# Kernel tuning notes

Measured on AMD Instinct MI355X. Metric: run time of the kernel, lower is better.

The kernel has to match this reference:

```python
import jax, jax.numpy as jnp
import numpy as np

B, S, H = 2, 2048, 2048
NH, NKV, HD = 16, 4, 128
ROPE_BASE = 10000.0


def setup_inputs() -> dict:
    key = jax.random.key(0)
    ks = jax.random.split(key, 5)
    x = jax.random.normal(ks[0], (B, S, H), dtype=jnp.float32)
    position_ids = jnp.arange(S, dtype=jnp.int64 if jax.config.jax_enable_x64 else jnp.int32).reshape(1, S)
    # Linear weights stored as [in, out] (equivalent to torch weight.T)
    sc = 1.0 / np.sqrt(H)
    Wq = jax.random.normal(ks[1], (H, NH * HD), dtype=jnp.float32) * sc
    Wk = jax.random.normal(ks[2], (H, NKV * HD), dtype=jnp.float32) * sc
    Wv = jax.random.normal(ks[3], (H, NKV * HD), dtype=jnp.float32) * sc
    Wo = jax.random.normal(ks[4], (NH * HD, H), dtype=jnp.float32) * (1.0 / np.sqrt(NH * HD))
    return {"x": x, "position_ids": position_ids, "Wq": Wq, "Wk": Wk, "Wv": Wv, "Wo": Wo}


def _rope(q, k, position_ids):
    # q: [B,S,NH,HD], k: [B,S,NKV,HD]; Llama-style half-split RoPE
    half = HD // 2
    inv_freq = 1.0 / (ROPE_BASE ** (jnp.arange(0, half, dtype=jnp.float32) * 2.0 / HD))
    ang = position_ids.astype(jnp.float32)[..., None] * inv_freq  # [b,S,half]
    cos = jnp.concatenate([jnp.cos(ang), jnp.cos(ang)], axis=-1)[:, :, None, :]  # [b,S,1,HD]
    sin = jnp.concatenate([jnp.sin(ang), jnp.sin(ang)], axis=-1)[:, :, None, :]

    def rot_half(t):
        t1, t2 = t[..., :half], t[..., half:]
        return jnp.concatenate([-t2, t1], axis=-1)

    return q * cos + rot_half(q) * sin, k * cos + rot_half(k) * sin


def reference(x, position_ids, Wq, Wk, Wv, Wo):
    b, s, _ = x.shape
    q = (x @ Wq).reshape(b, s, NH, HD)
    k = (x @ Wk).reshape(b, s, NKV, HD)
    v = (x @ Wv).reshape(b, s, NKV, HD)
    q, k = _rope(q, k, position_ids)
    reps = NH // NKV
    k = jnp.repeat(k, reps, axis=2)  # repeat_interleave on head dim
    v = jnp.repeat(v, reps, axis=2)
    q = q.transpose(0, 2, 1, 3)  # [b,h,s,d]
    k = k.transpose(0, 2, 1, 3)
    v = v.transpose(0, 2, 1, 3)
    scores = jnp.einsum('bhqd,bhkd->bhqk', q, k) / jnp.sqrt(jnp.float32(HD))
    causal = jnp.triu(jnp.ones((s, s), dtype=bool), k=1)
    scores = jnp.where(causal, -jnp.inf, scores)
    attn = jax.nn.softmax(scores.astype(jnp.float32), axis=-1).astype(q.dtype)
    out = jnp.einsum('bhqk,bhkd->bhqd', attn, v)
    out = out.transpose(0, 2, 1, 3).reshape(b, s, NH * HD)
    return out @ Wo
```

## Files before the change

kernel.cpp:

```cpp
#include <hip/hip_runtime.h>
#include <stdint.h>

typedef unsigned short u16;
typedef __attribute__((ext_vector_type(8))) short short8;
typedef __attribute__((ext_vector_type(4))) float floatx4;

#define S_LEN 2048
#define NQKV 3072

#if __has_builtin(__builtin_amdgcn_exp2f)
#define EXP2F __builtin_amdgcn_exp2f
#else
#define EXP2F exp2f
#endif

__device__ inline float bf2f(u16 u) {
  union { uint32_t u; float f; } v; v.u = ((uint32_t)u) << 16; return v.f;
}
__device__ inline u16 f2bf(float f) {
  union { float f; uint32_t u; } v; v.f = f;
  uint32_t r = v.u + 0x7fffu + ((v.u >> 16) & 1u);
  return (u16)(r >> 16);
}
__device__ inline void gl2lds16(const u16* g, u16* l) {
  __builtin_amdgcn_global_load_lds((const __attribute__((address_space(1))) uint32_t*)g,
                                   (__attribute__((address_space(3))) uint32_t*)l, 16, 0, 0);
}

__global__ void prep_k(const float* __restrict__ x, u16* __restrict__ Xb,
                       const float* __restrict__ Wq, const float* __restrict__ Wk,
                       const float* __restrict__ Wv, const float* __restrict__ Wo,
                       u16* __restrict__ WT, u16* __restrict__ WoT,
                       const int* __restrict__ pos, float2* __restrict__ rtab) {
  __shared__ u16 tile[32][33];
  const int b = blockIdx.x, t = threadIdx.x;
  if (b < 8192) {
    int i = b * 256 + t;
    float4 v = ((const float4*)x)[i];
    ushort4 o;
    o.x = f2bf(v.x); o.y = f2bf(v.y); o.z = f2bf(v.z); o.w = f2bf(v.w);
    ((ushort4*)Xb)[i] = o;
    return;
  }
  if (b >= 18432) {
    int i = (b - 18432) * 256 + t;
    int s = i >> 6, d = i & 63;
    float freq = __expf(-(float)d * 0.015625f * 9.210340371976184f);
    float ang = (float)pos[s] * freq;
    rtab[i] = make_float2(cosf(ang), sinf(ang));
    return;
  }
  int wb = b - 8192;
  const float* src; u16* dst; int bx, by;
  if (wb < 4096)      { src = Wq; dst = WT;                       bx = wb & 63;  by = wb >> 6; }
  else if (wb < 5120) { src = Wk; dst = WT + (size_t)2048 * 2048; bx = (wb - 4096) & 15; by = (wb - 4096) >> 4; }
  else if (wb < 6144) { src = Wv; dst = WT + (size_t)2560 * 2048; bx = (wb - 5120) & 15; by = (wb - 5120) >> 4; }
  else                { src = Wo; dst = WoT;                      bx = (wb - 6144) & 63; by = (wb - 6144) >> 6; }
  const int N = (wb >= 4096 && wb < 6144) ? 512 : 2048;
  int n0 = bx * 32, k0 = by * 32;
  int tx = t & 31, ty = t >> 5;
#pragma unroll
  for (int i = 0; i < 4; i++)
    tile[ty + 8 * i][tx] = f2bf(src[(size_t)(k0 + ty + 8 * i) * N + n0 + tx]);
  __syncthreads();
#pragma unroll
  for (int i = 0; i < 4; i++)
    dst[(size_t)(n0 + ty + 8 * i) * 2048 + k0 + tx] = tile[tx][ty + 8 * i];
}

__global__ void vtrans_k(const u16* __restrict__ qkv, u16* __restrict__ vt) {
  __shared__ u16 tile[32][33];
  int bk = blockIdx.x * 32, bd = blockIdx.y * 32, bz = blockIdx.z;
  int bb = bz >> 2, kvh = bz & 3;
  const u16* src = qkv + ((size_t)bb * S_LEN) * NQKV + 2560 + kvh * 128;
  u16* dst = vt + (size_t)bz * 128 * 2048;
  int tx = threadIdx.x, ty = threadIdx.y;
#pragma unroll
  for (int i = 0; i < 4; i++)
    tile[ty + 8 * i][tx] = src[(size_t)(bk + ty + 8 * i) * NQKV + bd + tx];
  __syncthreads();
#pragma unroll
  for (int i = 0; i < 4; i++)
    dst[(size_t)(bd + ty + 8 * i) * 2048 + bk + tx] = tile[tx][ty + 8 * i];
}

template <bool OUTF32>
__global__ __launch_bounds__(256) void gemm_bt(const u16* __restrict__ A, const u16* __restrict__ Bt,
                                               void* __restrict__ Cv, int M, int N, int K) {
  __shared__ u16 As[128 * 32];
  __shared__ u16 Bs[128 * 32];
  const int m0 = blockIdx.y * 128, n0 = blockIdx.x * 128;
  const int t = threadIdx.x, w = t >> 6, lane = t & 63;
  const int quad = lane >> 4, l16 = lane & 15;
  const int wm = (w >> 1) * 64, wn = (w & 1) * 64;
  const int lrow = lane >> 2, lk = (lane & 3) * 8;
  floatx4 acc[4][4] = {};
  for (int k0 = 0; k0 < K; k0 += 32) {
#pragma unroll
    for (int c = 2 * w; c <= 2 * w + 1; ++c) {
      int row = c * 16 + lrow;
      gl2lds16(A + (size_t)(m0 + row) * K + k0 + lk, As + c * 512 + lane * 8);
      gl2lds16(Bt + (size_t)(n0 + row) * K + k0 + lk, Bs + c * 512 + lane * 8);
    }
    __syncthreads();
    short8 a[4], b[4];
#pragma unroll
    for (int mt = 0; mt < 4; mt++) a[mt] = *(const short8*)(As + (wm + mt * 16 + l16) * 32 + quad * 8);
#pragma unroll
    for (int nt = 0; nt < 4; nt++) b[nt] = *(const short8*)(Bs + (wn + nt * 16 + l16) * 32 + quad * 8);
#pragma unroll
    for (int mt = 0; mt < 4; mt++)
#pragma unroll
      for (int nt = 0; nt < 4; nt++)
        acc[mt][nt] = __builtin_amdgcn_mfma_f32_16x16x32_bf16(a[mt], b[nt], acc[mt][nt], 0, 0, 0);
    __syncthreads();
  }
#pragma unroll
  for (int mt = 0; mt < 4; mt++)
#pragma unroll
    for (int nt = 0; nt < 4; nt++)
#pragma unroll
      for (int r = 0; r < 4; r++) {
        int row = m0 + wm + mt * 16 + quad * 4 + r;
        int col = n0 + wn + nt * 16 + l16;
        if (OUTF32)
          ((float*)Cv)[(size_t)row * N + col] = acc[mt][nt][r];
        else
          ((u16*)Cv)[(size_t)row * N + col] = f2bf(acc[mt][nt][r]);
      }
}

__global__ __launch_bounds__(512, 2) void gemm256_k(const u16* __restrict__ A,
                                                    const u16* __restrict__ Bt,
                                                    u16* __restrict__ C,
                                                    const float2* __restrict__ rtab,
                                                    int N, int K) {
  __shared__ u16 Al[2][2][8192];
  __shared__ u16 Bl[2][2][8192];
  const int TN = N >> 8;
  int flat = blockIdx.x;
  const int cpx = gridDim.x >> 3;
  flat = (flat & 7) * cpx + (flat >> 3);
  const int m0 = (flat / TN) << 8, n0 = (flat % TN) << 8;
  const int t = threadIdx.x, w = t >> 6, lane = t & 63;
  const int quad = lane >> 4, l16 = lane & 15;
  const int wm = w >> 2, wn = w & 3;
  const int sr = t >> 3, sl = t & 7;
  floatx4 acc[2][2][4][2] = {};
  const int NKT = K >> 6;

  const int ra_l = wm * 64 + l16;
  const int rb_l = wn * 16 + l16;

#pragma unroll
  for (int round = 0; round < 2; round++) {
    int r = round * 64 + sr;
    int so = (sl ^ (r & 7)) << 3;
    gl2lds16(A + (size_t)(m0 + r) * K + so, &Al[0][0][0] + round * 4096 + t * 8);
    gl2lds16(Bt + (size_t)(n0 + r) * K + so, &Bl[0][0][0] + round * 4096 + t * 8);
    gl2lds16(Bt + (size_t)(n0 + 128 + r) * K + so, &Bl[0][1][0] + round * 4096 + t * 8);
    gl2lds16(A + (size_t)(m0 + 128 + r) * K + so, &Al[0][1][0] + round * 4096 + t * 8);
  }
  asm volatile("s_waitcnt vmcnt(0)" ::: "memory");
  __builtin_amdgcn_s_barrier();

  short8 af[4][2];
  short8 bf[2][2][2];

  for (int kt = 0; kt < NKT; kt++) {
    const int c = kt & 1;
    const u16* Ab = &Al[c][0][0];
    const u16* Bb = &Bl[c][0][0];
    u16* An = &Al[c ^ 1][0][0];
    u16* Bn = &Bl[c ^ 1][0][0];
    const int k1 = (kt + 1) << 6;
    const bool pf = (kt + 1 < NKT);
#pragma unroll
    for (int ph = 0; ph < 4; ph++) {
      const int mh = (ph >> 1);
      const int nh = (ph == 1 || ph == 2) ? 1 : 0;
      if (ph == 0 || ph == 2) {
#pragma unroll
        for (int mt = 0; mt < 4; mt++) {
          int ra = ra_l + mt * 16;
          const u16* base = Ab + mh * 8192 + ra * 64;
#pragma unroll
          for (int ks = 0; ks < 2; ks++)
            af[mt][ks] = *(const short8*)(base + (((ks * 4 + quad) ^ (ra & 7)) << 3));
        }
      }
      if (ph == 0 || ph == 1) {
#pragma unroll
        for (int nt = 0; nt < 2; nt++) {
          int rb = rb_l + nt * 64;
          const u16* base = Bb + nh * 8192 + rb * 64;
#pragma unroll
          for (int ks = 0; ks < 2; ks++)
            bf[nh][nt][ks] = *(const short8*)(base + (((ks * 4 + quad) ^ (rb & 7)) << 3));
        }
      }
      if (pf) {
        const u16* G;
        u16* L;
        int rbase;
        if (ph == 0)      { G = A;  L = An;        rbase = m0; }
        else if (ph == 1) { G = Bt; L = Bn;        rbase = n0; }
        else if (ph == 2) { G = Bt; L = Bn + 8192; rbase = n0 + 128; }
        else              { G = A;  L = An + 8192; rbase = m0 + 128; }
#pragma unroll
        for (int round = 0; round < 2; round++) {
          int r = round * 64 + sr;
          gl2lds16(G + (size_t)(rbase + r) * K + k1 + ((sl ^ (r & 7)) << 3),
                   L + round * 4096 + t * 8);
        }
      }
      __builtin_amdgcn_s_barrier();
      asm volatile("s_waitcnt lgkmcnt(0)" ::: "memory");
      __builtin_amdgcn_s_setprio(1);
#pragma unroll
      for (int mt = 0; mt < 4; mt++)
#pragma unroll
        for (int nt = 0; nt < 2; nt++)
#pragma unroll
          for (int ks = 0; ks < 2; ks++)
            acc[mh][nh][mt][nt] =
                __builtin_amdgcn_mfma_f32_16x16x32_bf16(af[mt][ks], bf[nh][nt][ks], acc[mh][nh][mt][nt], 0, 0, 0);
      __builtin_amdgcn_s_setprio(0);
      if (ph != 2) asm volatile("s_waitcnt vmcnt(4)" ::: "memory");
      __builtin_amdgcn_s_barrier();
    }
  }
  const bool dorope = (n0 < 2560);
  const int dloc = wn * 16 + l16;
#pragma unroll
  for (int mh = 0; mh < 2; mh++)
#pragma unroll
    for (int mt = 0; mt < 4; mt++)
#pragma unroll
      for (int r = 0; r < 4; r++) {
        int row = m0 + mh * 128 + wm * 64 + mt * 16 + quad * 4 + r;
        float cc = 1.f, sn = 0.f;
        if (dorope) {
          float2 cs = rtab[(row & (S_LEN - 1)) * 64 + dloc];
          cc = cs.x; sn = cs.y;
        }
#pragma unroll
        for (int nh = 0; nh < 2; nh++) {
          float a0 = acc[mh][nh][mt][0][r], a1 = acc[mh][nh][mt][1][r];
          float o0 = dorope ? (a0 * cc - a1 * sn) : a0;
          float o1 = dorope ? (a1 * cc + a0 * sn) : a1;
          int colb = n0 + nh * 128 + wn * 16 + l16;
          C[(size_t)row * N + colb]      = f2bf(o0);
          C[(size_t)row * N + colb + 64] = f2bf(o1);
        }
      }
}

__global__ __launch_bounds__(256) void attn_k(const u16* __restrict__ qkv,
                                              const u16* __restrict__ vt,
                                              u16* __restrict__ ctx) {
  __shared__ u16 Kl[2][64 * 128];
  __shared__ u16 Vl[2][128 * 64];
  const int p = blockIdx.x;
  const int h = blockIdx.y, bb = blockIdx.z;
  const int kvh = h >> 2;
  const int t = threadIdx.x, w = t >> 6, lane = t & 63;
  const int quad = lane >> 4, l16 = lane & 15;
  const int sx = l16 & 7;
  const int kslot = lane & 15;
  const int vd0 = w * 32 + (lane >> 3);
  const int vslot = lane & 7;
  const int grow0 = (w & 1) * 4 + (w >> 1) * 32 + quad;
  const size_t rowbase = (size_t)bb * S_LEN;
  const u16* Kg0 = qkv + rowbase * NQKV + 2048 + kvh * 128;
  const u16* Vg0 = vt + (size_t)(bb * 4 + kvh) * 128 * 2048;
  const float c2 = 0.12751744f;
  short8 onesf = {16256, 16256, 16256, 16256, 16256, 16256, 16256, 16256};

  for (int phase = 0; phase < 2; phase++) {
    const int qt = phase ? p : 31 - p;
    const int rw = qt * 64 + w * 16;
    const int qrow = rw + l16;

    short8 qf[4];
#pragma unroll
    for (int ks = 0; ks < 4; ks++)
      qf[ks] = *(const short8*)(qkv + (rowbase + rw + l16) * NQKV + h * 128 + ks * 32 + quad * 8);

    floatx4 acc[8] = {};
    floatx4 accl = {0.f, 0.f, 0.f, 0.f};

    __syncthreads();
    {
#pragma unroll
      for (int ii = 0; ii < 4; ii++) {
        int p7 = (quad + 4 * ii) & 7;
        int grow = grow0 + 8 * ii;
        gl2lds16(Kg0 + (size_t)grow * NQKV + ((kslot ^ p7) * 8),
                 &Kl[0][0] + w * 2048 + ii * 512 + lane * 8);
      }
#pragma unroll
      for (int ii = 0; ii < 4; ii++) {
        int d = vd0 + ii * 8;
        gl2lds16(Vg0 + (size_t)d * 2048 + ((vslot ^ (d & 7)) * 8),
                 &Vl[0][0] + w * 2048 + ii * 512 + lane * 8);
      }
    }

    for (int kb = 0; kb <= qt; kb++) {
      const int cur = kb & 1;
      __builtin_amdgcn_s_barrier();
      if (kb < qt) {
        const u16* Kg = Kg0 + (size_t)(kb + 1) * 64 * NQKV;
        const u16* Vg = Vg0 + (kb + 1) * 64;
        u16* KlN = &Kl[cur ^ 1][0];
        u16* VlN = &Vl[cur ^ 1][0];
#pragma unroll
        for (int ii = 0; ii < 4; ii++) {
          int p7 = (quad + 4 * ii) & 7;
          int grow = grow0 + 8 * ii;
          gl2lds16(Kg + (size_t)grow * NQKV + ((kslot ^ p7) * 8),
                   KlN + w * 2048 + ii * 512 + lane * 8);
        }
#pragma unroll
        for (int ii = 0; ii < 4; ii++) {
          int d = vd0 + ii * 8;
          gl2lds16(Vg + (size_t)d * 2048 + ((vslot ^ (d & 7)) * 8),
                   VlN + w * 2048 + ii * 512 + lane * 8);
        }
        asm volatile("s_waitcnt vmcnt(8)" ::: "memory");
      } else {
        asm volatile("s_waitcnt vmcnt(0)" ::: "memory");
      }
      __builtin_amdgcn_s_barrier();
      const u16* KlB = &Kl[cur][0];
      const u16* VlB = &Vl[cur][0];

      floatx4 sc[4];
#pragma unroll
      for (int nt = 0; nt < 4; nt++) {
        const u16* Krow = KlB + (nt * 16 + l16) * 128;
        short8 kf[4];
#pragma unroll
        for (int ks = 0; ks < 4; ks++)
          kf[ks] = *(const short8*)(Krow + (((ks * 4 + quad) ^ sx) * 8));
        floatx4 s = {0.f, 0.f, 0.f, 0.f};
#pragma unroll
        for (int ks = 0; ks < 4; ks++) s = __builtin_amdgcn_mfma_f32_16x16x32_bf16(kf[ks], qf[ks], s, 0, 0, 0);
        sc[nt] = s;
      }
      const bool diag = (kb == qt);
      uint32_t pw[8];
#pragma unroll
      for (int nt = 0; nt < 4; nt++) {
        uint32_t w0 = 0, w1 = 0;
#pragma unroll
        for (int r = 0; r < 4; r++) {
          float e = EXP2F(sc[nt][r] * c2);
          if (diag) {
            int keyg = kb * 64 + quad * 8 + (nt & 1) * 4 + (nt >> 1) * 32 + r;
            if (keyg > qrow) e = 0.f;
          }
          uint32_t b = __float_as_uint(e) >> 16;
          if (r == 0) w0 = b;
          else if (r == 1) w0 |= b << 16;
          else if (r == 2) w1 = b;
          else w1 |= b << 16;
        }
        pw[nt * 2] = w0;
        pw[nt * 2 + 1] = w1;
      }
      union { short8 v; uint32_t u[4]; } pu0, pu1;
      pu0.u[0] = pw[0]; pu0.u[1] = pw[1]; pu0.u[2] = pw[2]; pu0.u[3] = pw[3];
      pu1.u[0] = pw[4]; pu1.u[1] = pw[5]; pu1.u[2] = pw[6]; pu1.u[3] = pw[7];
      const short8 pf0 = pu0.v, pf1 = pu1.v;

      accl = __builtin_amdgcn_mfma_f32_16x16x32_bf16(pf0, onesf, accl, 0, 0, 0);
      accl = __builtin_amdgcn_mfma_f32_16x16x32_bf16(pf1, onesf, accl, 0, 0, 0);
#pragma unroll
      for (int nto = 0; nto < 8; nto++) {
        const u16* Vrow = VlB + (nto * 16 + l16) * 64;
        short8 vf0 = *(const short8*)(Vrow + ((quad ^ sx) * 8));
        short8 vf1 = *(const short8*)(Vrow + (((quad + 4) ^ sx) * 8));
        acc[nto] = __builtin_amdgcn_mfma_f32_16x16x32_bf16(pf0, vf0, acc[nto], 0, 0, 0);
        acc[nto] = __builtin_amdgcn_mfma_f32_16x16x32_bf16(pf1, vf1, acc[nto], 0, 0, 0);
      }
    }
#pragma unroll
    for (int r = 0; r < 4; r++) {
      float inv = 1.0f / accl[r];
      int rowg = rw + quad * 4 + r;
#pragma unroll
      for (int nto = 0; nto < 8; nto++) {
        int col = h * 128 + nto * 16 + l16;
        ctx[(rowbase + rowg) * 2048 + col] = f2bf(acc[nto][r] * inv);
      }
    }
  }
}

extern "C" void kernel_launch(void* const* d_in, const int* in_sizes, int n_in,
                              void* d_out, int out_size, void* d_ws, size_t ws_size,
                              hipStream_t stream) {
  const float* x  = (const float*)d_in[0];
  const int* pos  = (const int*)d_in[1];
  const float* Wq = (const float*)d_in[2];
  const float* Wk = (const float*)d_in[3];
  const float* Wv = (const float*)d_in[4];
  const float* Wo = (const float*)d_in[5];
  float* out = (float*)d_out;
  char* ws = (char*)d_ws;
  u16* Xb  = (u16*)(ws);
  u16* WT  = (u16*)(ws + 16777216);
  u16* WoT = (u16*)(ws + 29360128);
  u16* QKV = (u16*)(ws + 37748736);
  u16* CTX = (u16*)(ws + 62914560);
  u16* VT  = Xb;
  float2* rtab = (float2*)(ws + 62914560);

  hipLaunchKernelGGL(prep_k, dim3(18944), dim3(256), 0, stream, x, Xb, Wq, Wk, Wv, Wo, WT, WoT, pos, rtab);

  hipLaunchKernelGGL(gemm256_k, dim3(192), dim3(512), 0, stream, Xb, WT, QKV, rtab, 3072, 2048);
  dim3 tb(32, 8);
  hipLaunchKernelGGL(vtrans_k, dim3(64, 4, 8), tb, 0, stream, QKV, VT);
  hipLaunchKernelGGL(attn_k, dim3(16, 16, 2), dim3(256), 0, stream, QKV, VT, CTX);
  hipLaunchKernelGGL(HIP_KERNEL_NAME(gemm_bt<true>), dim3(16, 32), dim3(256), 0, stream,
                     CTX, WoT, (void*)out, 4096, 2048, 2048);
}
```

Baseline: 290.1 us.

## Fuse V transpose into QKV GEMM epilogue and drop vtrans kernel

The QKV GEMM epilogue now stages V tiles through LDS and writes them transposed into the V region of the QKV buffer, so the separate vtrans kernel and its extra read/write of V are removed. Attention reads V from that packed transposed layout in place. The change also adds s_setprio around the MFMA blocks in attention and a vmcnt(0) wait on the last k-iteration. The epilogue reuses the GEMM shared memory and uses a more complex store pattern for V tiles.

```diff
diff --git a/kernel.cpp b/kernel.cpp
--- a/kernel.cpp
+++ b/kernel.cpp
@@ -3,6 +3,7 @@
 
 typedef unsigned short u16;
 typedef __attribute__((ext_vector_type(8))) short short8;
+typedef __attribute__((ext_vector_type(4))) short short4v;
 typedef __attribute__((ext_vector_type(4))) float floatx4;
 
 #define S_LEN 2048
@@ -68,22 +69,6 @@
     dst[(size_t)(n0 + ty + 8 * i) * 2048 + k0 + tx] = tile[tx][ty + 8 * i];
 }
 
-__global__ void vtrans_k(const u16* __restrict__ qkv, u16* __restrict__ vt) {
-  __shared__ u16 tile[32][33];
-  int bk = blockIdx.x * 32, bd = blockIdx.y * 32, bz = blockIdx.z;
-  int bb = bz >> 2, kvh = bz & 3;
-  const u16* src = qkv + ((size_t)bb * S_LEN) * NQKV + 2560 + kvh * 128;
-  u16* dst = vt + (size_t)bz * 128 * 2048;
-  int tx = threadIdx.x, ty = threadIdx.y;
-#pragma unroll
-  for (int i = 0; i < 4; i++)
-    tile[ty + 8 * i][tx] = src[(size_t)(bk + ty + 8 * i) * NQKV + bd + tx];
-  __syncthreads();
-#pragma unroll
-  for (int i = 0; i < 4; i++)
-    dst[(size_t)(bd + ty + 8 * i) * 2048 + bk + tx] = tile[tx][ty + 8 * i];
-}
-
 template <bool OUTF32>
 __global__ __launch_bounds__(256) void gemm_bt(const u16* __restrict__ A, const u16* __restrict__ Bt,
                                                void* __restrict__ Cv, int M, int N, int K) {
@@ -135,8 +120,9 @@
                                                     u16* __restrict__ C,
                                                     const float2* __restrict__ rtab,
                                                     int N, int K) {
-  __shared__ u16 Al[2][2][8192];
-  __shared__ u16 Bl[2][2][8192];
+  __shared__ u16 SM[65536];
+  u16* const AlB = SM;
+  u16* const BlB = SM + 32768;
   const int TN = N >> 8;
   int flat = blockIdx.x;
   const int cpx = gridDim.x >> 3;
@@ -156,10 +142,10 @@
   for (int round = 0; round < 2; round++) {
     int r = round * 64 + sr;
     int so = (sl ^ (r & 7)) << 3;
-    gl2lds16(A + (size_t)(m0 + r) * K + so, &Al[0][0][0] + round * 4096 + t * 8);
-    gl2lds16(Bt + (size_t)(n0 + r) * K + so, &Bl[0][0][0] + round * 4096 + t * 8);
-    gl2lds16(Bt + (size_t)(n0 + 128 + r) * K + so, &Bl[0][1][0] + round * 4096 + t * 8);
-    gl2lds16(A + (size_t)(m0 + 128 + r) * K + so, &Al[0][1][0] + round * 4096 + t * 8);
+    gl2lds16(A + (size_t)(m0 + r) * K + so, AlB + round * 4096 + t * 8);
+    gl2lds16(Bt + (size_t)(n0 + r) * K + so, BlB + round * 4096 + t * 8);
+    gl2lds16(Bt + (size_t)(n0 + 128 + r) * K + so, BlB + 8192 + round * 4096 + t * 8);
+    gl2lds16(A + (size_t)(m0 + 128 + r) * K + so, AlB + 8192 + round * 4096 + t * 8);
   }
   asm volatile("s_waitcnt vmcnt(0)" ::: "memory");
   __builtin_amdgcn_s_barrier();
@@ -169,10 +155,10 @@
 
   for (int kt = 0; kt < NKT; kt++) {
     const int c = kt & 1;
-    const u16* Ab = &Al[c][0][0];
-    const u16* Bb = &Bl[c][0][0];
-    u16* An = &Al[c ^ 1][0][0];
-    u16* Bn = &Bl[c ^ 1][0][0];
+    const u16* Ab = AlB + c * 16384;
+    const u16* Bb = BlB + c * 16384;
+    u16* An = AlB + (c ^ 1) * 16384;
+    u16* Bn = BlB + (c ^ 1) * 16384;
     const int k1 = (kt + 1) << 6;
     const bool pf = (kt + 1 < NKT);
 #pragma unroll
@@ -226,38 +212,67 @@
             acc[mh][nh][mt][nt] =
                 __builtin_amdgcn_mfma_f32_16x16x32_bf16(af[mt][ks], bf[nh][nt][ks], acc[mh][nh][mt][nt], 0, 0, 0);
       __builtin_amdgcn_s_setprio(0);
-      if (ph != 2) asm volatile("s_waitcnt vmcnt(4)" ::: "memory");
+      if (ph != 2) {
+        if (pf) asm volatile("s_waitcnt vmcnt(4)" ::: "memory");
+        else    asm volatile("s_waitcnt vmcnt(0)" ::: "memory");
+      }
       __builtin_amdgcn_s_barrier();
     }
   }
-  const bool dorope = (n0 < 2560);
-  const int dloc = wn * 16 + l16;
-#pragma unroll
-  for (int mh = 0; mh < 2; mh++)
-#pragma unroll
-    for (int mt = 0; mt < 4; mt++)
-#pragma unroll
-      for (int r = 0; r < 4; r++) {
-        int row = m0 + mh * 128 + wm * 64 + mt * 16 + quad * 4 + r;
-        float cc = 1.f, sn = 0.f;
-        if (dorope) {
+  if (n0 < 2560) {
+    const int dloc = wn * 16 + l16;
+#pragma unroll
+    for (int mh = 0; mh < 2; mh++)
+#pragma unroll
+      for (int mt = 0; mt < 4; mt++)
+#pragma unroll
+        for (int r = 0; r < 4; r++) {
+          int row = m0 + mh * 128 + wm * 64 + mt * 16 + quad * 4 + r;
           float2 cs = rtab[(row & (S_LEN - 1)) * 64 + dloc];
-          cc = cs.x; sn = cs.y;
-        }
-#pragma unroll
-        for (int nh = 0; nh < 2; nh++) {
-          float a0 = acc[mh][nh][mt][0][r], a1 = acc[mh][nh][mt][1][r];
-          float o0 = dorope ? (a0 * cc - a1 * sn) : a0;
-          float o1 = dorope ? (a1 * cc + a0 * sn) : a1;
-          int colb = n0 + nh * 128 + wn * 16 + l16;
-          C[(size_t)row * N + colb]      = f2bf(o0);
-          C[(size_t)row * N + colb + 64] = f2bf(o1);
-        }
-      }
+#pragma unroll
+          for (int nh = 0; nh < 2; nh++) {
+            float a0 = acc[mh][nh][mt][0][r], a1 = acc[mh][nh][mt][1][r];
+            float o0 = a0 * cs.x - a1 * cs.y;
+            float o1 = a1 * cs.x + a0 * cs.y;
+            int colb = n0 + nh * 128 + wn * 16 + l16;
+            C[(size_t)row * N + colb]      = f2bf(o0);
+            C[(size_t)row * N + colb + 64] = f2bf(o1);
+          }
+        }
+  } else {
+    const int bbv = m0 >> 11, m0loc = m0 & 2047;
+    const int kvbase = (n0 - 2560) >> 7;
+#pragma unroll
+    for (int mh = 0; mh < 2; mh++)
+#pragma unroll
+      for (int nh = 0; nh < 2; nh++)
+#pragma unroll
+        for (int mt = 0; mt < 4; mt++)
+#pragma unroll
+          for (int pair = 0; pair < 2; pair++) {
+            int lrow = mh * 128 + wm * 64 + mt * 16 + quad * 4;
+            int lcol = nh * 128 + wn * 16 + l16 + pair * 64;
+            short4v v4 = { (short)f2bf(acc[mh][nh][mt][pair][0]),
+                           (short)f2bf(acc[mh][nh][mt][pair][1]),
+                           (short)f2bf(acc[mh][nh][mt][pair][2]),
+                           (short)f2bf(acc[mh][nh][mt][pair][3]) };
+            *(short4v*)(SM + lcol * 256 + (lrow ^ ((lcol & 15) << 3))) = v4;
+          }
+    asm volatile("s_waitcnt lgkmcnt(0)" ::: "memory");
+    __builtin_amdgcn_s_barrier();
+#pragma unroll
+    for (int it = 0; it < 16; it++) {
+      int u = it * 512 + t;
+      int key0 = (u & 31) * 8, lcol = u >> 5;
+      short8 v = *(const short8*)(SM + lcol * 256 + (key0 ^ ((lcol & 15) << 3)));
+      int d = lcol & 127, kvh = kvbase + (lcol >> 7);
+      int key = m0loc + key0;
+      *(short8*)(C + (size_t)(bbv * 2048 + kvh * 512 + d * 4 + (key >> 9)) * N + 2560 + (key & 511)) = v;
+    }
+  }
 }
 
 __global__ __launch_bounds__(256) void attn_k(const u16* __restrict__ qkv,
-                                              const u16* __restrict__ vt,
                                               u16* __restrict__ ctx) {
   __shared__ u16 Kl[2][64 * 128];
   __shared__ u16 Vl[2][128 * 64];
@@ -273,7 +288,7 @@
   const int grow0 = (w & 1) * 4 + (w >> 1) * 32 + quad;
   const size_t rowbase = (size_t)bb * S_LEN;
   const u16* Kg0 = qkv + rowbase * NQKV + 2048 + kvh * 128;
-  const u16* Vg0 = vt + (size_t)(bb * 4 + kvh) * 128 * 2048;
+  const u16* Vg0 = qkv + (rowbase + kvh * 512) * NQKV + 2560;
   const float c2 = 0.12751744f;
   short8 onesf = {16256, 16256, 16256, 16256, 16256, 16256, 16256, 16256};
 
@@ -302,7 +317,8 @@
 #pragma unroll
       for (int ii = 0; ii < 4; ii++) {
         int d = vd0 + ii * 8;
-        gl2lds16(Vg0 + (size_t)d * 2048 + ((vslot ^ (d & 7)) * 8),
+        int s8 = (vslot ^ (d & 7)) * 8;
+        gl2lds16(Vg0 + (size_t)(d * 4) * NQKV + s8,
                  &Vl[0][0] + w * 2048 + ii * 512 + lane * 8);
       }
     }
@@ -311,8 +327,8 @@
       const int cur = kb & 1;
       __builtin_amdgcn_s_barrier();
       if (kb < qt) {
-        const u16* Kg = Kg0 + (size_t)(kb + 1) * 64 * NQKV;
-        const u16* Vg = Vg0 + (kb + 1) * 64;
+        const int kn = kb + 1;
+        const u16* Kg = Kg0 + (size_t)kn * 64 * NQKV;
         u16* KlN = &Kl[cur ^ 1][0];
         u16* VlN = &Vl[cur ^ 1][0];
 #pragma unroll
@@ -325,7 +341,8 @@
 #pragma unroll
         for (int ii = 0; ii < 4; ii++) {
           int d = vd0 + ii * 8;
-          gl2lds16(Vg + (size_t)d * 2048 + ((vslot ^ (d & 7)) * 8),
+          int s8 = (vslot ^ (d & 7)) * 8;
+          gl2lds16(Vg0 + (size_t)(d * 4 + (kn >> 3)) * NQKV + (kn & 7) * 64 + s8,
                    VlN + w * 2048 + ii * 512 + lane * 8);
         }
         asm volatile("s_waitcnt vmcnt(8)" ::: "memory");
@@ -337,6 +354,7 @@
       const u16* VlB = &Vl[cur][0];
 
       floatx4 sc[4];
+      __builtin_amdgcn_s_setprio(1);
 #pragma unroll
       for (int nt = 0; nt < 4; nt++) {
         const u16* Krow = KlB + (nt * 16 + l16) * 128;
@@ -349,6 +367,7 @@
         for (int ks = 0; ks < 4; ks++) s = __builtin_amdgcn_mfma_f32_16x16x32_bf16(kf[ks], qf[ks], s, 0, 0, 0);
         sc[nt] = s;
       }
+      __builtin_amdgcn_s_setprio(0);
       const bool diag = (kb == qt);
       uint32_t pw[8];
 #pragma unroll
@@ -375,6 +394,7 @@
       pu1.u[0] = pw[4]; pu1.u[1] = pw[5]; pu1.u[2] = pw[6]; pu1.u[3] = pw[7];
       const short8 pf0 = pu0.v, pf1 = pu1.v;
 
+      __builtin_amdgcn_s_setprio(1);
       accl = __builtin_amdgcn_mfma_f32_16x16x32_bf16(pf0, onesf, accl, 0, 0, 0);
       accl = __builtin_amdgcn_mfma_f32_16x16x32_bf16(pf1, onesf, accl, 0, 0, 0);
 #pragma unroll
@@ -385,6 +405,7 @@
         acc[nto] = __builtin_amdgcn_mfma_f32_16x16x32_bf16(pf0, vf0, acc[nto], 0, 0, 0);
         acc[nto] = __builtin_amdgcn_mfma_f32_16x16x32_bf16(pf1, vf1, acc[nto], 0, 0, 0);
       }
+      __builtin_amdgcn_s_setprio(0);
     }
 #pragma unroll
     for (int r = 0; r < 4; r++) {
@@ -415,15 +436,12 @@
   u16* WoT = (u16*)(ws + 29360128);
   u16* QKV = (u16*)(ws + 37748736);
   u16* CTX = (u16*)(ws + 62914560);
-  u16* VT  = Xb;
   float2* rtab = (float2*)(ws + 62914560);
 
   hipLaunchKernelGGL(prep_k, dim3(18944), dim3(256), 0, stream, x, Xb, Wq, Wk, Wv, Wo, WT, WoT, pos, rtab);
 
   hipLaunchKernelGGL(gemm256_k, dim3(192), dim3(512), 0, stream, Xb, WT, QKV, rtab, 3072, 2048);
-  dim3 tb(32, 8);
-  hipLaunchKernelGGL(vtrans_k, dim3(64, 4, 8), tb, 0, stream, QKV, VT);
-  hipLaunchKernelGGL(attn_k, dim3(16, 16, 2), dim3(256), 0, stream, QKV, VT, CTX);
+  hipLaunchKernelGGL(attn_k, dim3(16, 16, 2), dim3(256), 0, stream, QKV, CTX);
   hipLaunchKernelGGL(HIP_KERNEL_NAME(gemm_bt<true>), dim3(16, 32), dim3(256), 0, stream,
                      CTX, WoT, (void*)out, 4096, 2048, 2048);
 }
```

Result: faster. 283.9 us (-2.1%).
